# Kernel optimization log

Measured on AMD Instinct MI355X. Metric: run time of the kernel, lower is better.

Reference implementation:

```python
import jax, jax.numpy as jnp
import numpy as np

N = 100000       # nodes
E = 1600000      # edges (avg degree 16)
C_IN = 128
C_OUT = 64
C_HID = 2 * C_OUT  # 128, matches GCNEncoder's 2*out_channels hidden width


def setup_inputs() -> dict:
    key = jax.random.key(0)
    k1, k2, k3, k4 = jax.random.split(key, 4)
    x = jax.random.normal(k1, (N, C_IN), dtype=jnp.float32)
    edge_index = jax.random.randint(k2, (2, E), 0, N, dtype=jnp.int64)
    # Glorot-ish scale for the linear weights (PyG GCNConv uses glorot init)
    W1 = jax.random.normal(k3, (C_IN, C_HID), dtype=jnp.float32) / np.sqrt(C_IN)
    b1 = jnp.zeros((C_HID,), dtype=jnp.float32)
    W2 = jax.random.normal(k4, (C_HID, C_OUT), dtype=jnp.float32) / np.sqrt(C_HID)
    b2 = jnp.zeros((C_OUT,), dtype=jnp.float32)
    return {"x": x, "edge_index": edge_index, "W1": W1, "b1": b1, "W2": W2, "b2": b2}


def _gcn_conv(x, src, dst, norm_e, self_norm, W, b):
    # GCNConv: out = D^{-1/2} (A + I) D^{-1/2} (x @ W) + b
    h = x @ W                                   # [N, C'] transform first (cheaper)
    msg = h[src] * norm_e[:, None]              # [E, C'] gather + edge normalization
    agg = jax.ops.segment_sum(msg, dst, num_segments=N)  # scatter-add over targets
    return agg + self_norm[:, None] * h + b     # self-loop term + bias


def reference(x, edge_index, W1, b1, W2, b2):
    src, dst = edge_index[0], edge_index[1]
    # degrees on A + I (self-loops added), identical for both layers
    deg = jax.ops.segment_sum(jnp.ones((E,), jnp.float32), dst, num_segments=N) + 1.0
    dinv = jax.lax.rsqrt(deg)                   # deg >= 1, no zero-guard needed
    norm_e = dinv[src] * dinv[dst]              # [E]
    self_norm = dinv * dinv                     # [N]

    h = _gcn_conv(x, src, dst, norm_e, self_norm, W1, b1)
    h = jax.nn.relu(h)
    return _gcn_conv(h, src, dst, norm_e, self_norm, W2, b2)
```

## Files before the change

kernel.cpp:

```cpp
#include <hip/hip_runtime.h>
#include <hip/hip_fp16.h>

#define NN   100000
#define NE   1600000
#define CIN  128
#define CHID 128
#define COUT 64

#define NPB  256
#define NB   391
#define NBLK 128
#define CHUNK ((NE + NBLK - 1) / NBLK)

typedef _Float16 f16x8 __attribute__((ext_vector_type(8)));
typedef float    f32x4 __attribute__((ext_vector_type(4)));

#define NTILE 782
#define GGRID 512

__global__ __launch_bounds__(512) void k_passA(const int* __restrict__ dst,
                                               int* __restrict__ tab) {
  __shared__ int hist[NB];
  int tid = threadIdx.x;
  for (int t = tid; t < NB; t += 512) hist[t] = 0;
  __syncthreads();
  int i0 = blockIdx.x * CHUNK;
  int i1 = min(i0 + CHUNK, NE);
  for (int i = i0 + tid; i < i1; i += 512)
    atomicAdd(&hist[((unsigned)dst[i]) >> 8], 1);
  __syncthreads();
  for (int t = tid; t < NB; t += 512)
    tab[t * NBLK + blockIdx.x] = hist[t];
}

__global__ __launch_bounds__(512) void k_bscan(const int* __restrict__ tab,
                                               int* __restrict__ bb) {
  __shared__ int s[512];
  int t = threadIdx.x;
  int v = 0;
  if (t < NB) {
    const int* row = tab + t * NBLK;
#pragma unroll 8
    for (int k = 0; k < NBLK; k++) v += row[k];
  }
  s[t] = v;
  __syncthreads();
  for (int off = 1; off < 512; off <<= 1) {
    int u = (t >= off) ? s[t - off] : 0;
    __syncthreads();
    s[t] += u;
    __syncthreads();
  }
  if (t < NB) bb[t] = s[t] - v;
  if (t == 0) bb[NB] = NE;
}

__global__ __launch_bounds__(128) void k_tabscan(int* __restrict__ tab,
                                                 const int* __restrict__ bb) {
  __shared__ int s[128];
  int b = blockIdx.x, t = threadIdx.x;
  int v = tab[b * NBLK + t];
  s[t] = v;
  __syncthreads();
  for (int off = 1; off < 128; off <<= 1) {
    int u = (t >= off) ? s[t - off] : 0;
    __syncthreads();
    s[t] += u;
    __syncthreads();
  }
  tab[b * NBLK + t] = bb[b] + s[t] - v;
}

__global__ __launch_bounds__(512) void k_passB(const int* __restrict__ src,
                                               const int* __restrict__ dst,
                                               const int* __restrict__ tab,
                                               int* __restrict__ barr) {
  __shared__ int cur[NB];
  int tid = threadIdx.x;
  for (int t = tid; t < NB; t += 512) cur[t] = tab[t * NBLK + blockIdx.x];
  __syncthreads();
  int i0 = blockIdx.x * CHUNK;
  int i1 = min(i0 + CHUNK, NE);
  for (int i = i0 + tid; i < i1; i += 512) {
    int d = dst[i];
    unsigned b = ((unsigned)d) >> 8;
    int p = atomicAdd(&cur[b], 1);
    barr[p] = (src[i] << 8) | (d & 255);
  }
}

__global__ __launch_bounds__(256) void k_l2(const int* __restrict__ barr,
                                            const int* __restrict__ bb,
                                            int* __restrict__ csr,
                                            int* __restrict__ rs,
                                            float* __restrict__ dinv) {
  __shared__ int lcnt[NPB];
  __shared__ int lcur[NPB];
  int b = blockIdx.x, t = threadIdx.x;
  int e0 = bb[b], e1 = bb[b + 1];
  lcnt[t] = 0;
  __syncthreads();
  for (int i = e0 + t; i < e1; i += 256) atomicAdd(&lcnt[barr[i] & 255], 1);
  __syncthreads();
  int v = lcnt[t];
  lcur[t] = v;
  __syncthreads();
  for (int off = 1; off < 256; off <<= 1) {
    int u = (t >= off) ? lcur[t - off] : 0;
    __syncthreads();
    lcur[t] += u;
    __syncthreads();
  }
  int ex = lcur[t] - v;
  __syncthreads();
  lcur[t] = e0 + ex;
  int g = b * NPB + t;
  if (g <= NN) rs[g] = e0 + ex;
  if (g < NN) dinv[g] = rsqrtf((float)v + 1.0f);
  __syncthreads();
  for (int i = e0 + t; i < e1; i += 256) {
    int w = barr[i];
    int p = atomicAdd(&lcur[w & 255], 1);
    csr[p] = ((unsigned)w) >> 8;
  }
}

__global__ __launch_bounds__(256, 2) void k_gemm1(const float* __restrict__ X,
                                                  const float* __restrict__ W,
                                                  const float* __restrict__ dinv,
                                                  __half* __restrict__ G) {
  __shared__ _Float16 Wt[128][128];
  int tid = threadIdx.x;
  for (int i = tid; i < 128 * 32; i += 256) {
    int k = i >> 5, c4 = (i & 31) << 2;
    float4 v = ((const float4*)W)[i];
    Wt[c4 + 0][k] = (_Float16)v.x;
    Wt[c4 + 1][k] = (_Float16)v.y;
    Wt[c4 + 2][k] = (_Float16)v.z;
    Wt[c4 + 3][k] = (_Float16)v.w;
  }
  __syncthreads();
  int wv = tid >> 6, lane = tid & 63;
  int l15 = lane & 15, g = lane >> 4;

  f16x8 wf[8][4];
#pragma unroll
  for (int cf = 0; cf < 8; cf++)
#pragma unroll
    for (int ks = 0; ks < 4; ks++)
      wf[cf][ks] = *(const f16x8*)&Wt[cf * 16 + l15][ks * 32 + g * 8];

  for (int t = blockIdx.x; t < NTILE; t += GGRID) {
    int rowbase = t * 128 + wv * 32;
    f32x4 acc[2][8];
#pragma unroll
    for (int i = 0; i < 2; i++)
#pragma unroll
      for (int j = 0; j < 8; j++) acc[i][j] = (f32x4){0.f, 0.f, 0.f, 0.f};

    int r0 = min(rowbase + l15, NN - 1);
    int r1 = min(rowbase + 16 + l15, NN - 1);
    const float* p0 = X + (size_t)r0 * CIN + g * 8;
    const float* p1 = X + (size_t)r1 * CIN + g * 8;

    float4 u0a = *(const float4*)p0, u0b = *(const float4*)(p0 + 4);
    float4 u1a = *(const float4*)p1, u1b = *(const float4*)(p1 + 4);

#pragma unroll
    for (int ks = 0; ks < 4; ks++) {
      f16x8 xa, xb;
      xa[0] = (_Float16)u0a.x; xa[1] = (_Float16)u0a.y;
      xa[2] = (_Float16)u0a.z; xa[3] = (_Float16)u0a.w;
      xa[4] = (_Float16)u0b.x; xa[5] = (_Float16)u0b.y;
      xa[6] = (_Float16)u0b.z; xa[7] = (_Float16)u0b.w;
      xb[0] = (_Float16)u1a.x; xb[1] = (_Float16)u1a.y;
      xb[2] = (_Float16)u1a.z; xb[3] = (_Float16)u1a.w;
      xb[4] = (_Float16)u1b.x; xb[5] = (_Float16)u1b.y;
      xb[6] = (_Float16)u1b.z; xb[7] = (_Float16)u1b.w;
      if (ks < 3) {
        int o = (ks + 1) * 32;
        u0a = *(const float4*)(p0 + o); u0b = *(const float4*)(p0 + o + 4);
        u1a = *(const float4*)(p1 + o); u1b = *(const float4*)(p1 + o + 4);
      }
#pragma unroll
      for (int cf = 0; cf < 8; cf++) {
        acc[0][cf] = __builtin_amdgcn_mfma_f32_16x16x32_f16(wf[cf][ks], xa, acc[0][cf], 0, 0, 0);
        acc[1][cf] = __builtin_amdgcn_mfma_f32_16x16x32_f16(wf[cf][ks], xb, acc[1][cf], 0, 0, 0);
      }
    }

#pragma unroll
    for (int rf = 0; rf < 2; rf++) {
      int row = rowbase + rf * 16 + l15;
      if (row < NN) {
        float dn = dinv[row];
#pragma unroll
        for (int cf = 0; cf < 8; cf++) {
          int col = cf * 16 + g * 4;
          __half2 h0 = __half2(__float2half(dn * acc[rf][cf][0]),
                               __float2half(dn * acc[rf][cf][1]));
          __half2 h1 = __half2(__float2half(dn * acc[rf][cf][2]),
                               __float2half(dn * acc[rf][cf][3]));
          uint2 s;
          s.x = *(unsigned*)&h0;
          s.y = *(unsigned*)&h1;
          *(uint2*)(G + (size_t)row * CHID + col) = s;
        }
      }
    }
  }
}

__global__ __launch_bounds__(256, 2) void k_gemm2(const __half* __restrict__ X,
                                                  const float* __restrict__ W,
                                                  const float* __restrict__ dinv,
                                                  __half* __restrict__ G) {
  __shared__ _Float16 Wt[64][128];
  int tid = threadIdx.x;
  for (int i = tid; i < 128 * 16; i += 256) {
    int k = i >> 4, c4 = (i & 15) << 2;
    float4 v = ((const float4*)W)[i];
    Wt[c4 + 0][k] = (_Float16)v.x;
    Wt[c4 + 1][k] = (_Float16)v.y;
    Wt[c4 + 2][k] = (_Float16)v.z;
    Wt[c4 + 3][k] = (_Float16)v.w;
  }
  __syncthreads();
  int wv = tid >> 6, lane = tid & 63;
  int l15 = lane & 15, g = lane >> 4;

  f16x8 wf[4][4];
#pragma unroll
  for (int cf = 0; cf < 4; cf++)
#pragma unroll
    for (int ks = 0; ks < 4; ks++)
      wf[cf][ks] = *(const f16x8*)&Wt[cf * 16 + l15][ks * 32 + g * 8];

  for (int t = blockIdx.x; t < NTILE; t += GGRID) {
    int rowbase = t * 128 + wv * 32;
    f32x4 acc[2][4];
#pragma unroll
    for (int i = 0; i < 2; i++)
#pragma unroll
      for (int j = 0; j < 4; j++) acc[i][j] = (f32x4){0.f, 0.f, 0.f, 0.f};

    int r0 = min(rowbase + l15, NN - 1);
    int r1 = min(rowbase + 16 + l15, NN - 1);
    const _Float16* p0 = (const _Float16*)X + (size_t)r0 * CHID + g * 8;
    const _Float16* p1 = (const _Float16*)X + (size_t)r1 * CHID + g * 8;

    f16x8 xa = *(const f16x8*)p0;
    f16x8 xb = *(const f16x8*)p1;

#pragma unroll
    for (int ks = 0; ks < 4; ks++) {
      f16x8 ca = xa, cb = xb;
      if (ks < 3) {
        int o = (ks + 1) * 32;
        xa = *(const f16x8*)(p0 + o);
        xb = *(const f16x8*)(p1 + o);
      }
#pragma unroll
      for (int cf = 0; cf < 4; cf++) {
        acc[0][cf] = __builtin_amdgcn_mfma_f32_16x16x32_f16(wf[cf][ks], ca, acc[0][cf], 0, 0, 0);
        acc[1][cf] = __builtin_amdgcn_mfma_f32_16x16x32_f16(wf[cf][ks], cb, acc[1][cf], 0, 0, 0);
      }
    }

#pragma unroll
    for (int rf = 0; rf < 2; rf++) {
      int row = rowbase + rf * 16 + l15;
      if (row < NN) {
        float dn = dinv[row];
#pragma unroll
        for (int cf = 0; cf < 4; cf++) {
          int col = cf * 16 + g * 4;
          __half2 h0 = __half2(__float2half(dn * acc[rf][cf][0]),
                               __float2half(dn * acc[rf][cf][1]));
          __half2 h1 = __half2(__float2half(dn * acc[rf][cf][2]),
                               __float2half(dn * acc[rf][cf][3]));
          uint2 s;
          s.x = *(unsigned*)&h0;
          s.y = *(unsigned*)&h1;
          *(uint2*)(G + (size_t)row * COUT + col) = s;
        }
      }
    }
  }
}

__global__ __launch_bounds__(256) void k_agg1(const __half* __restrict__ g,
                                              const int* __restrict__ rs,
                                              const int* __restrict__ csr,
                                              const float* __restrict__ dinv,
                                              const float* __restrict__ b,
                                              __half* __restrict__ o) {
  int wid = (blockIdx.x * blockDim.x + threadIdx.x) >> 6;
  int lane = threadIdx.x & 63;
  if (wid >= NN) return;
  const __half2* gp = (const __half2*)g;

  float2 self = __half22float2(gp[(size_t)wid * 64 + lane]);
  float a0x = self.x, a0y = self.y;
  float a1x = 0.f, a1y = 0.f, a2x = 0.f, a2y = 0.f, a3x = 0.f, a3y = 0.f;

  int e0 = rs[wid];
  int deg = rs[wid + 1] - e0;
  for (int base = 0; base < deg; base += 64) {
    int rem = deg - base;
    int m = rem < 64 ? rem : 64;
    int idx = (lane < m) ? csr[e0 + base + lane] : 0;
    int j = 0;
    for (; j + 3 < m; j += 4) {
      int s0 = __shfl(idx, j);
      int s1 = __shfl(idx, j + 1);
      int s2 = __shfl(idx, j + 2);
      int s3 = __shfl(idx, j + 3);
      float2 v0 = __half22float2(gp[(size_t)s0 * 64 + lane]);
      float2 v1 = __half22float2(gp[(size_t)s1 * 64 + lane]);
      float2 v2 = __half22float2(gp[(size_t)s2 * 64 + lane]);
      float2 v3 = __half22float2(gp[(size_t)s3 * 64 + lane]);
      a0x += v0.x; a0y += v0.y;
      a1x += v1.x; a1y += v1.y;
      a2x += v2.x; a2y += v2.y;
      a3x += v3.x; a3y += v3.y;
    }
    for (; j < m; j++) {
      int s = __shfl(idx, j);
      float2 v = __half22float2(gp[(size_t)s * 64 + lane]);
      a0x += v.x; a0y += v.y;
    }
  }
  float ax = (a0x + a1x) + (a2x + a3x);
  float ay = (a0y + a1y) + (a2y + a3y);
  float dn = dinv[wid];
  float2 bb = ((const float2*)b)[lane];
  float rx = fmaxf(fmaf(dn, ax, bb.x), 0.f);
  float ry = fmaxf(fmaf(dn, ay, bb.y), 0.f);
  ((__half2*)o)[(size_t)wid * 64 + lane] =
      __half2(__float2half(rx), __float2half(ry));
}

__global__ __launch_bounds__(256) void k_agg2(const __half* __restrict__ g,
                                              const int* __restrict__ rs,
                                              const int* __restrict__ csr,
                                              const float* __restrict__ dinv,
                                              const float* __restrict__ b,
                                              float* __restrict__ o) {
  int wid = (blockIdx.x * blockDim.x + threadIdx.x) >> 6;
  int lane = threadIdx.x & 63;
  if (wid >= NN) return;

  float a0 = __half2float(g[(size_t)wid * COUT + lane]);
  float a1 = 0.f, a2 = 0.f, a3 = 0.f;

  int e0 = rs[wid];
  int deg = rs[wid + 1] - e0;
  for (int base = 0; base < deg; base += 64) {
    int rem = deg - base;
    int m = rem < 64 ? rem : 64;
    int idx = (lane < m) ? csr[e0 + base + lane] : 0;
    int j = 0;
    for (; j + 3 < m; j += 4) {
      int s0 = __shfl(idx, j);
      int s1 = __shfl(idx, j + 1);
      int s2 = __shfl(idx, j + 2);
      int s3 = __shfl(idx, j + 3);
      a0 += __half2float(g[(size_t)s0 * COUT + lane]);
      a1 += __half2float(g[(size_t)s1 * COUT + lane]);
      a2 += __half2float(g[(size_t)s2 * COUT + lane]);
      a3 += __half2float(g[(size_t)s3 * COUT + lane]);
    }
    for (; j < m; j++) {
      int s = __shfl(idx, j);
      a0 += __half2float(g[(size_t)s * COUT + lane]);
    }
  }
  float acc = (a0 + a1) + (a2 + a3);
  o[(size_t)wid * COUT + lane] = fmaf(dinv[wid], acc, b[lane]);
}


extern "C" void kernel_launch(void* const* d_in, const int* in_sizes, int n_in,
                              void* d_out, int out_size, void* d_ws, size_t ws_size,
                              hipStream_t stream) {
  const float* x  = (const float*)d_in[0];
  const int*   ei = (const int*)d_in[1];
  const float* W1 = (const float*)d_in[2];
  const float* b1 = (const float*)d_in[3];
  const float* W2 = (const float*)d_in[4];
  const float* b2 = (const float*)d_in[5];
  float* out = (float*)d_out;

  const int* esrc = ei;
  const int* edst = ei + NE;

  char* p = (char*)d_ws;
  __half* g1 = (__half*)p;    p += (size_t)NN * CHID * 2;
  __half* o1 = (__half*)p;    p += (size_t)NN * CHID * 2;
  __half* g2 = (__half*)p;    p += (size_t)NN * COUT * 2;
  int* rs  = (int*)p;         p += (size_t)(NN + 1) * 4;
  float* dinv = (float*)p;    p += (size_t)NN * 4;
  int* tab = (int*)p;         p += (size_t)NB * NBLK * 4;
  int* bb  = (int*)p;         p += (size_t)(NB + 1) * 4;
  int* barr = (int*)p;        p += (size_t)NE * 4;
  int* csr = (int*)p;         p += (size_t)NE * 4;

  hipLaunchKernelGGL(k_passA, dim3(NBLK), dim3(512), 0, stream, edst, tab);
  hipLaunchKernelGGL(k_bscan, dim3(1), dim3(512), 0, stream, tab, bb);
  hipLaunchKernelGGL(k_tabscan, dim3(NB), dim3(128), 0, stream, tab, bb);
  hipLaunchKernelGGL(k_passB, dim3(NBLK), dim3(512), 0, stream, esrc, edst, tab, barr);
  hipLaunchKernelGGL(k_l2, dim3(NB), dim3(256), 0, stream, barr, bb, csr, rs, dinv);

  hipLaunchKernelGGL(k_gemm1, dim3(GGRID), dim3(256), 0, stream, x, W1, dinv, g1);
  hipLaunchKernelGGL(k_agg1, dim3((NN + 3) / 4), dim3(256), 0, stream, g1, rs, csr, dinv, b1, o1);

  hipLaunchKernelGGL(k_gemm2, dim3(GGRID), dim3(256), 0, stream, o1, W2, dinv, g2);
  hipLaunchKernelGGL(k_agg2, dim3((NN + 3) / 4), dim3(256), 0, stream, g2, rs, csr, dinv, b2, out);
}
```

Before: 219.9 us.

## Pad CSR rows to multiples of eight and gather with 16-byte per-lane loads

Each node's CSR row is padded to a multiple of eight entries, with padding slots pointing at an extra zero row appended to the feature buffers. The aggregation kernels then split each wavefront into lane groups that each gather a full neighbour row with uint4 loads, processing several edges in parallel, and reduce across groups with shuffles. This replaces per-lane half2/half loads and the shuffle-broadcast index loop, so memory requests are wider and there is no tail loop. In exchange it adds padding traffic (up to seven dummy gathers per node), extra CSR space, and a cross-group reduction.

New measurement: 224.3 us (median of 3 runs). 1.02x slower.

```diff
diff --git a/kernel.cpp b/kernel.cpp
--- a/kernel.cpp
+++ b/kernel.cpp
@@ -11,12 +11,19 @@
 #define NB   391
 #define NBLK 128
 #define CHUNK ((NE + NBLK - 1) / NBLK)
+#define BPAD 2048
 
 typedef _Float16 f16x8 __attribute__((ext_vector_type(8)));
 typedef float    f32x4 __attribute__((ext_vector_type(4)));
 
 #define NTILE 782
 #define GGRID 512
+
+__global__ void k_zrow(__half* __restrict__ g1, __half* __restrict__ g2) {
+  int t = threadIdx.x;
+  if (t < 128) g1[(size_t)NN * CHID + t] = __float2half(0.f);
+  if (t < 64)  g2[(size_t)NN * COUT + t] = __float2half(0.f);
+}
 
 __global__ __launch_bounds__(512) void k_passA(const int* __restrict__ dst,
                                                int* __restrict__ tab) {
@@ -93,6 +100,7 @@
                                             const int* __restrict__ bb,
                                             int* __restrict__ csr,
                                             int* __restrict__ rs,
+                                            int* __restrict__ re,
                                             float* __restrict__ dinv) {
   __shared__ int lcnt[NPB];
   __shared__ int lcur[NPB];
@@ -103,7 +111,8 @@
   for (int i = e0 + t; i < e1; i += 256) atomicAdd(&lcnt[barr[i] & 255], 1);
   __syncthreads();
   int v = lcnt[t];
-  lcur[t] = v;
+  int pv = (v + 7) & ~7;
+  lcur[t] = pv;
   __syncthreads();
   for (int off = 1; off < 256; off <<= 1) {
     int u = (t >= off) ? lcur[t - off] : 0;
@@ -111,12 +120,17 @@
     lcur[t] += u;
     __syncthreads();
   }
-  int ex = lcur[t] - v;
-  __syncthreads();
-  lcur[t] = e0 + ex;
+  int pex = lcur[t] - pv;
+  int start = e0 + b * BPAD + pex;
   int g = b * NPB + t;
-  if (g <= NN) rs[g] = e0 + ex;
-  if (g < NN) dinv[g] = rsqrtf((float)v + 1.0f);
+  if (g < NN) {
+    rs[g] = start;
+    re[g] = start + pv;
+    dinv[g] = rsqrtf((float)v + 1.0f);
+  }
+  __syncthreads();
+  lcur[t] = start;
+  for (int k = v; k < pv; k++) csr[start + k] = NN;
   __syncthreads();
   for (int i = e0 + t; i < e1; i += 256) {
     int w = barr[i];
@@ -289,95 +303,118 @@
   }
 }
 
+#define ACC8(A, V)                                                  \
+  {                                                                 \
+    float2 f;                                                       \
+    f = __half22float2(*(__half2*)&(V).x); A[0] += f.x; A[1] += f.y; \
+    f = __half22float2(*(__half2*)&(V).y); A[2] += f.x; A[3] += f.y; \
+    f = __half22float2(*(__half2*)&(V).z); A[4] += f.x; A[5] += f.y; \
+    f = __half22float2(*(__half2*)&(V).w); A[6] += f.x; A[7] += f.y; \
+  }
+
 __global__ __launch_bounds__(256) void k_agg1(const __half* __restrict__ g,
                                               const int* __restrict__ rs,
+                                              const int* __restrict__ re,
+                                              const float* __restrict__ dinv,
                                               const int* __restrict__ csr,
-                                              const float* __restrict__ dinv,
                                               const float* __restrict__ b,
                                               __half* __restrict__ o) {
   int wid = (blockIdx.x * blockDim.x + threadIdx.x) >> 6;
   int lane = threadIdx.x & 63;
   if (wid >= NN) return;
-  const __half2* gp = (const __half2*)g;
-
-  float2 self = __half22float2(gp[(size_t)wid * 64 + lane]);
-  float a0x = self.x, a0y = self.y;
-  float a1x = 0.f, a1y = 0.f, a2x = 0.f, a2y = 0.f, a3x = 0.f, a3y = 0.f;
-
-  int e0 = rs[wid];
-  int deg = rs[wid + 1] - e0;
-  for (int base = 0; base < deg; base += 64) {
-    int rem = deg - base;
-    int m = rem < 64 ? rem : 64;
-    int idx = (lane < m) ? csr[e0 + base + lane] : 0;
-    int j = 0;
-    for (; j + 3 < m; j += 4) {
-      int s0 = __shfl(idx, j);
-      int s1 = __shfl(idx, j + 1);
-      int s2 = __shfl(idx, j + 2);
-      int s3 = __shfl(idx, j + 3);
-      float2 v0 = __half22float2(gp[(size_t)s0 * 64 + lane]);
-      float2 v1 = __half22float2(gp[(size_t)s1 * 64 + lane]);
-      float2 v2 = __half22float2(gp[(size_t)s2 * 64 + lane]);
-      float2 v3 = __half22float2(gp[(size_t)s3 * 64 + lane]);
-      a0x += v0.x; a0y += v0.y;
-      a1x += v1.x; a1y += v1.y;
-      a2x += v2.x; a2y += v2.y;
-      a3x += v3.x; a3y += v3.y;
-    }
-    for (; j < m; j++) {
-      int s = __shfl(idx, j);
-      float2 v = __half22float2(gp[(size_t)s * 64 + lane]);
-      a0x += v.x; a0y += v.y;
-    }
-  }
-  float ax = (a0x + a1x) + (a2x + a3x);
-  float ay = (a0y + a1y) + (a2y + a3y);
-  float dn = dinv[wid];
-  float2 bb = ((const float2*)b)[lane];
-  float rx = fmaxf(fmaf(dn, ax, bb.x), 0.f);
-  float ry = fmaxf(fmaf(dn, ay, bb.y), 0.f);
-  ((__half2*)o)[(size_t)wid * 64 + lane] =
-      __half2(__float2half(rx), __float2half(ry));
+  int q = lane >> 4, ql = lane & 15;
+  const uint4* gp = (const uint4*)g;
+
+  float aA[8] = {0.f, 0.f, 0.f, 0.f, 0.f, 0.f, 0.f, 0.f};
+  float aB[8] = {0.f, 0.f, 0.f, 0.f, 0.f, 0.f, 0.f, 0.f};
+
+  if (q == 0) {
+    uint4 v = gp[(size_t)wid * 16 + ql];
+    ACC8(aA, v);
+  }
+
+  int i0 = rs[wid], i1 = re[wid];
+  for (int i = i0; i < i1; i += 8) {
+    int sA = csr[i + q];
+    int sB = csr[i + 4 + q];
+    uint4 vA = gp[(size_t)sA * 16 + ql];
+    uint4 vB = gp[(size_t)sB * 16 + ql];
+    ACC8(aA, vA);
+    ACC8(aB, vB);
+  }
+
+  float r[8];
+#pragma unroll
+  for (int c = 0; c < 8; c++) {
+    float t = aA[c] + aB[c];
+    t += __shfl_xor(t, 16);
+    t += __shfl_xor(t, 32);
+    r[c] = t;
+  }
+  if (q == 0) {
+    float dn = dinv[wid];
+    float4 b0 = *(const float4*)(b + 8 * ql);
+    float4 b1 = *(const float4*)(b + 8 * ql + 4);
+    __half2 h[4];
+    h[0] = __half2(__float2half(fmaxf(fmaf(dn, r[0], b0.x), 0.f)),
+                   __float2half(fmaxf(fmaf(dn, r[1], b0.y), 0.f)));
+    h[1] = __half2(__float2half(fmaxf(fmaf(dn, r[2], b0.z), 0.f)),
+                   __float2half(fmaxf(fmaf(dn, r[3], b0.w), 0.f)));
+    h[2] = __half2(__float2half(fmaxf(fmaf(dn, r[4], b1.x), 0.f)),
+                   __float2half(fmaxf(fmaf(dn, r[5], b1.y), 0.f)));
+    h[3] = __half2(__float2half(fmaxf(fmaf(dn, r[6], b1.z), 0.f)),
+                   __float2half(fmaxf(fmaf(dn, r[7], b1.w), 0.f)));
+    *(uint4*)(o + (size_t)wid * CHID + 8 * ql) = *(uint4*)h;
+  }
 }
 
 __global__ __launch_bounds__(256) void k_agg2(const __half* __restrict__ g,
                                               const int* __restrict__ rs,
+                                              const int* __restrict__ re,
+                                              const float* __restrict__ dinv,
                                               const int* __restrict__ csr,
-                                              const float* __restrict__ dinv,
                                               const float* __restrict__ b,
                                               float* __restrict__ o) {
   int wid = (blockIdx.x * blockDim.x + threadIdx.x) >> 6;
   int lane = threadIdx.x & 63;
   if (wid >= NN) return;
-
-  float a0 = __half2float(g[(size_t)wid * COUT + lane]);
-  float a1 = 0.f, a2 = 0.f, a3 = 0.f;
-
-  int e0 = rs[wid];
-  int deg = rs[wid + 1] - e0;
-  for (int base = 0; base < deg; base += 64) {
-    int rem = deg - base;
-    int m = rem < 64 ? rem : 64;
-    int idx = (lane < m) ? csr[e0 + base + lane] : 0;
-    int j = 0;
-    for (; j + 3 < m; j += 4) {
-      int s0 = __shfl(idx, j);
-      int s1 = __shfl(idx, j + 1);
-      int s2 = __shfl(idx, j + 2);
-      int s3 = __shfl(idx, j + 3);
-      a0 += __half2float(g[(size_t)s0 * COUT + lane]);
-      a1 += __half2float(g[(size_t)s1 * COUT + lane]);
-      a2 += __half2float(g[(size_t)s2 * COUT + lane]);
-      a3 += __half2float(g[(size_t)s3 * COUT + lane]);
-    }
-    for (; j < m; j++) {
-      int s = __shfl(idx, j);
-      a0 += __half2float(g[(size_t)s * COUT + lane]);
-    }
-  }
-  float acc = (a0 + a1) + (a2 + a3);
-  o[(size_t)wid * COUT + lane] = fmaf(dinv[wid], acc, b[lane]);
+  int g8 = lane >> 3, gl = lane & 7;
+  const uint4* gp = (const uint4*)g;
+
+  float aA[8] = {0.f, 0.f, 0.f, 0.f, 0.f, 0.f, 0.f, 0.f};
+
+  if (g8 == 0) {
+    uint4 v = gp[(size_t)wid * 8 + gl];
+    ACC8(aA, v);
+  }
+
+  int i0 = rs[wid], i1 = re[wid];
+  for (int i = i0; i < i1; i += 8) {
+    int s = csr[i + g8];
+    uint4 v = gp[(size_t)s * 8 + gl];
+    ACC8(aA, v);
+  }
+
+  float r[8];
+#pragma unroll
+  for (int c = 0; c < 8; c++) {
+    float t = aA[c];
+    t += __shfl_xor(t, 8);
+    t += __shfl_xor(t, 16);
+    t += __shfl_xor(t, 32);
+    r[c] = t;
+  }
+  if (g8 == 0) {
+    float dn = dinv[wid];
+    float4 b0 = *(const float4*)(b + 8 * gl);
+    float4 b1 = *(const float4*)(b + 8 * gl + 4);
+    float4 o0 = make_float4(fmaf(dn, r[0], b0.x), fmaf(dn, r[1], b0.y),
+                            fmaf(dn, r[2], b0.z), fmaf(dn, r[3], b0.w));
+    float4 o1v = make_float4(fmaf(dn, r[4], b1.x), fmaf(dn, r[5], b1.y),
+                             fmaf(dn, r[6], b1.z), fmaf(dn, r[7], b1.w));
+    *(float4*)(o + (size_t)wid * COUT + 8 * gl) = o0;
+    *(float4*)(o + (size_t)wid * COUT + 8 * gl + 4) = o1v;
+  }
 }
 
 
@@ -396,25 +433,28 @@
   const int* edst = ei + NE;
 
   char* p = (char*)d_ws;
-  __half* g1 = (__half*)p;    p += (size_t)NN * CHID * 2;
+  __half* g1 = (__half*)p;    p += (size_t)(NN + 1) * CHID * 2;
   __half* o1 = (__half*)p;    p += (size_t)NN * CHID * 2;
-  __half* g2 = (__half*)p;    p += (size_t)NN * COUT * 2;
-  int* rs  = (int*)p;         p += (size_t)(NN + 1) * 4;
+  __half* g2 = (__half*)p;    p += (size_t)(NN + 1) * COUT * 2;
+  int* rs  = (int*)p;         p += (size_t)NN * 4;
+  int* re  = (int*)p;         p += (size_t)NN * 4;
   float* dinv = (float*)p;    p += (size_t)NN * 4;
   int* tab = (int*)p;         p += (size_t)NB * NBLK * 4;
   int* bb  = (int*)p;         p += (size_t)(NB + 1) * 4;
   int* barr = (int*)p;        p += (size_t)NE * 4;
-  int* csr = (int*)p;         p += (size_t)NE * 4;
+  int* csr = (int*)p;         p += (size_t)(NE + NB * BPAD) * 4;
+
+  hipLaunchKernelGGL(k_zrow, dim3(1), dim3(128), 0, stream, g1, g2);
 
   hipLaunchKernelGGL(k_passA, dim3(NBLK), dim3(512), 0, stream, edst, tab);
   hipLaunchKernelGGL(k_bscan, dim3(1), dim3(512), 0, stream, tab, bb);
   hipLaunchKernelGGL(k_tabscan, dim3(NB), dim3(128), 0, stream, tab, bb);
   hipLaunchKernelGGL(k_passB, dim3(NBLK), dim3(512), 0, stream, esrc, edst, tab, barr);
-  hipLaunchKernelGGL(k_l2, dim3(NB), dim3(256), 0, stream, barr, bb, csr, rs, dinv);
+  hipLaunchKernelGGL(k_l2, dim3(NB), dim3(256), 0, stream, barr, bb, csr, rs, re, dinv);
 
   hipLaunchKernelGGL(k_gemm1, dim3(GGRID), dim3(256), 0, stream, x, W1, dinv, g1);
-  hipLaunchKernelGGL(k_agg1, dim3((NN + 3) / 4), dim3(256), 0, stream, g1, rs, csr, dinv, b1, o1);
+  hipLaunchKernelGGL(k_agg1, dim3((NN + 3) / 4), dim3(256), 0, stream, g1, rs, re, dinv, csr, b1, o1);
 
   hipLaunchKernelGGL(k_gemm2, dim3(GGRID), dim3(256), 0, stream, o1, W2, dinv, g2);
-  hipLaunchKernelGGL(k_agg2, dim3((NN + 3) / 4), dim3(256), 0, stream, g2, rs, csr, dinv, b2, out);
-}
+  hipLaunchKernelGGL(k_agg2, dim3((NN + 3) / 4), dim3(256), 0, stream, g2, rs, re, dinv, csr, b2, out);
+}
```
